# Kernel tuning notes

Hardware: AMD Instinct MI355X
Metric: run time of the kernel (lower is better)

The kernel has to match this reference:

```python
import jax, jax.numpy as jnp
import numpy as np

N = 1_600_000          # total points across all polylines
NUM_SEG = 100_000      # number of polylines (segments for scatter_max)
C_IN = 64
C_OUT = 64
NEG_SLOPE = 0.01       # F.leaky_relu default


def setup_inputs() -> dict:
    key = jax.random.key(0)
    k1, k2, k3, k4 = jax.random.split(key, 4)
    features = jax.random.normal(k1, (N, C_IN), dtype=jnp.float32)
    W = jax.random.normal(k2, (C_OUT, C_IN), dtype=jnp.float32) * (1.0 / np.sqrt(C_IN))
    b = jax.random.normal(k3, (C_OUT,), dtype=jnp.float32) * 0.01
    agg_indices = jax.random.randint(k4, (N,), 0, NUM_SEG, dtype=jnp.int32)
    return {"features": features, "W": W, "b": b, "agg_indices": agg_indices}


def reference(features, W, b, agg_indices):
    # fc: Linear(in_channels, out_channels)  -> [N, C_OUT]
    h = features @ W.T + b
    # leaky_relu (default negative_slope=0.01)
    h = jnp.where(h >= 0, h, NEG_SLOPE * h)
    # scatter_max over segments (dim=0): [NUM_SEG, C_OUT]
    agg = jax.ops.segment_max(h, agg_indices, num_segments=NUM_SEG)
    # guard against empty segments (-inf from segment_max); torch_scatter leaves them 0
    agg = jnp.where(jnp.isfinite(agg), agg, 0.0)
    # gather-broadcast and concat -> [N, 2*C_OUT]
    out = jnp.concatenate([h, agg[agg_indices]], axis=-1)
    return out, agg
```

## Files before the change

### kernel.cpp

```cpp
#include <hip/hip_runtime.h>
#include <stdint.h>

#define C 64
#define CAP 64

typedef __attribute__((ext_vector_type(8))) short short8v;
typedef __attribute__((ext_vector_type(4))) float f32x4;

static __device__ __forceinline__ short f2bf(float f) {
    unsigned u = __float_as_uint(f);
    unsigned r = (u + 0x7FFFu + ((u >> 16) & 1u)) >> 16;
    return (short)r;
}

static __device__ __forceinline__ short8v cvt8(f32x4 lo, f32x4 hi) {
    short8v v;
    v[0] = f2bf(lo[0]); v[1] = f2bf(lo[1]); v[2] = f2bf(lo[2]); v[3] = f2bf(lo[3]);
    v[4] = f2bf(hi[0]); v[5] = f2bf(hi[1]); v[6] = f2bf(hi[2]); v[7] = f2bf(hi[3]);
    return v;
}

__global__ __launch_bounds__(256) void k_gemm_fill(
    const float* __restrict__ feat, const float* __restrict__ W,
    const float* __restrict__ b, const int* __restrict__ idx,
    float* __restrict__ out, unsigned int* __restrict__ bucket, int N)
{
    const int lane = threadIdx.x & 63;
    const int gw   = blockIdx.x * (blockDim.x >> 6) + (threadIdx.x >> 6);
    const int nw   = gridDim.x * (blockDim.x >> 6);
    const int r    = lane & 15;
    const int q    = lane >> 4;

    short8v wf[4][2];
#pragma unroll
    for (int ct = 0; ct < 4; ++ct)
#pragma unroll
        for (int kh = 0; kh < 2; ++kh) {
            const float* src = W + (size_t)(ct * 16 + r) * C + kh * 32 + q * 8;
            wf[ct][kh] = cvt8(*(const f32x4*)src, *(const f32x4*)(src + 4));
        }
    float bias[4];
#pragma unroll
    for (int ct = 0; ct < 4; ++ct) bias[ct] = b[ct * 16 + r];

    const f32x4 zero = {0.f, 0.f, 0.f, 0.f};
    const int nTiles = N >> 5;

    for (int t = gw; t < nTiles; t += nw) {
        int rowid = t * 32 + lane;
        int seg   = (lane < 32) ? idx[rowid] : 0;

        const float* a0 = feat + ((size_t)t * 32 + r) * C + q * 8;
        const float* a1 = a0 + 16 * C;
        f32x4 l00 = *(const f32x4*)(a0);
        f32x4 l01 = *(const f32x4*)(a0 + 4);
        f32x4 l02 = *(const f32x4*)(a0 + 32);
        f32x4 l03 = *(const f32x4*)(a0 + 36);
        f32x4 l10 = *(const f32x4*)(a1);
        f32x4 l11 = *(const f32x4*)(a1 + 4);
        f32x4 l12 = *(const f32x4*)(a1 + 32);
        f32x4 l13 = *(const f32x4*)(a1 + 36);

        if (lane < 32) {
            unsigned int old = atomicAdd(&bucket[(size_t)seg * CAP], 1u);
            if (old < CAP - 1)
                bucket[(size_t)seg * CAP + 1 + old] = (unsigned int)rowid;
        }

        short8v A0k0 = cvt8(l00, l01), A0k1 = cvt8(l02, l03);
        short8v A1k0 = cvt8(l10, l11), A1k1 = cvt8(l12, l13);

        f32x4 d0[4], d1[4];
#pragma unroll
        for (int ct = 0; ct < 4; ++ct) {
            d0[ct] = __builtin_amdgcn_mfma_f32_16x16x32_bf16(A0k0, wf[ct][0], zero, 0, 0, 0);
            d0[ct] = __builtin_amdgcn_mfma_f32_16x16x32_bf16(A0k1, wf[ct][1], d0[ct], 0, 0, 0);
            d1[ct] = __builtin_amdgcn_mfma_f32_16x16x32_bf16(A1k0, wf[ct][0], zero, 0, 0, 0);
            d1[ct] = __builtin_amdgcn_mfma_f32_16x16x32_bf16(A1k1, wf[ct][1], d1[ct], 0, 0, 0);
        }

        const size_t row0 = (size_t)t * 32 + q * 4;
#pragma unroll
        for (int ct = 0; ct < 4; ++ct)
#pragma unroll
            for (int j = 0; j < 4; ++j) {
                float v0 = d0[ct][j] + bias[ct];
                v0 = fmaxf(v0, 0.01f * v0);
                out[(row0 + j) * (2 * C) + ct * 16 + r] = v0;
                float v1 = d1[ct][j] + bias[ct];
                v1 = fmaxf(v1, 0.01f * v1);
                out[(row0 + 16 + j) * (2 * C) + ct * 16 + r] = v1;
            }
    }
}

__global__ __launch_bounds__(256) void k_reduce_scatter(
    float* __restrict__ out, unsigned int* __restrict__ bucket, int nseg)
{
    const int lane = threadIdx.x & 63;
    const int seg  = blockIdx.x * (blockDim.x >> 6) + (threadIdx.x >> 6);
    if (seg >= nseg) return;

    unsigned int* brow = bucket + (size_t)seg * CAP;
    const unsigned int v = brow[lane];
    int cnt = __shfl((int)v, 0, 64);
    if (cnt > CAP - 1) cnt = CAP - 1;

    float acc = -INFINITY;
    for (int rr = 1; rr <= cnt; ++rr) {
        int row = __shfl((int)v, rr, 64);
        acc = fmaxf(acc, out[(size_t)row * (2 * C) + lane]);
    }
    if (cnt == 0) acc = 0.0f;

    ((float*)brow)[lane] = acc;

    for (int rr = 1; rr <= cnt; ++rr) {
        int row = __shfl((int)v, rr, 64);
        out[(size_t)row * (2 * C) + C + lane] = acc;
    }
}

extern "C" void kernel_launch(void* const* d_in, const int* in_sizes, int n_in,
                              void* d_out, int out_size, void* d_ws, size_t ws_size,
                              hipStream_t stream)
{
    (void)n_in; (void)d_ws; (void)ws_size;
    const float* feat = (const float*)d_in[0];
    const float* W    = (const float*)d_in[1];
    const float* b    = (const float*)d_in[2];
    const int*   idx  = (const int*)d_in[3];
    float* out = (float*)d_out;

    const int N    = in_sizes[0] / C;
    const int nseg = (out_size - N * 2 * C) / C;

    float* aggOut = out + (size_t)N * 2 * C;
    unsigned int* bucket = (unsigned int*)aggOut;

    hipMemsetAsync(aggOut, 0, (size_t)nseg * CAP * sizeof(unsigned int), stream);

    k_gemm_fill<<<2048, 256, 0, stream>>>(feat, W, b, idx, out, bucket, N);
    k_reduce_scatter<<<(nseg + 3) / 4, 256, 0, stream>>>(out, bucket, nseg);
}
```

Before: 471.8 us.

## Prefetch next GEMM tile, use nontemporal accesses, vectorize segment reduce with 4 rows per wave

The GEMM loop now software-prefetches the next tile's feature rows into registers while computing the current tile. Feature loads and output stores use nontemporal hints to limit cache pollution. The reduce/scatter kernel processes four rows per iteration, with each quarter-wave loading a float4 slice, and merges the partial maxima with xor shuffles. It then writes the broadcast aggregate as float4 stores. This cuts per-row load/store instruction count and latency, at the cost of more registers and redundant duplicate stores when the count is not a multiple of four.

```diff
diff --git a/kernel.cpp b/kernel.cpp
--- a/kernel.cpp
+++ b/kernel.cpp
@@ -19,6 +19,20 @@
     v[4] = f2bf(hi[0]); v[5] = f2bf(hi[1]); v[6] = f2bf(hi[2]); v[7] = f2bf(hi[3]);
     return v;
 }
+
+#define LOADA(t, L)                                                          \
+    {                                                                        \
+        const float* a0_ = feat + ((size_t)(t) * 32 + r) * C + q * 8;        \
+        const float* a1_ = a0_ + 16 * C;                                     \
+        L[0] = __builtin_nontemporal_load((const f32x4*)(a0_));              \
+        L[1] = __builtin_nontemporal_load((const f32x4*)(a0_ + 4));          \
+        L[2] = __builtin_nontemporal_load((const f32x4*)(a0_ + 32));         \
+        L[3] = __builtin_nontemporal_load((const f32x4*)(a0_ + 36));         \
+        L[4] = __builtin_nontemporal_load((const f32x4*)(a1_));              \
+        L[5] = __builtin_nontemporal_load((const f32x4*)(a1_ + 4));          \
+        L[6] = __builtin_nontemporal_load((const f32x4*)(a1_ + 32));         \
+        L[7] = __builtin_nontemporal_load((const f32x4*)(a1_ + 36));         \
+    }
 
 __global__ __launch_bounds__(256) void k_gemm_fill(
     const float* __restrict__ feat, const float* __restrict__ W,
@@ -46,20 +60,16 @@
     const f32x4 zero = {0.f, 0.f, 0.f, 0.f};
     const int nTiles = N >> 5;
 
-    for (int t = gw; t < nTiles; t += nw) {
-        int rowid = t * 32 + lane;
-        int seg   = (lane < 32) ? idx[rowid] : 0;
+    f32x4 cur[8], nxt[8];
+    int t = gw;
+    if (t < nTiles) LOADA(t, cur);
 
-        const float* a0 = feat + ((size_t)t * 32 + r) * C + q * 8;
-        const float* a1 = a0 + 16 * C;
-        f32x4 l00 = *(const f32x4*)(a0);
-        f32x4 l01 = *(const f32x4*)(a0 + 4);
-        f32x4 l02 = *(const f32x4*)(a0 + 32);
-        f32x4 l03 = *(const f32x4*)(a0 + 36);
-        f32x4 l10 = *(const f32x4*)(a1);
-        f32x4 l11 = *(const f32x4*)(a1 + 4);
-        f32x4 l12 = *(const f32x4*)(a1 + 32);
-        f32x4 l13 = *(const f32x4*)(a1 + 36);
+    for (; t < nTiles; t += nw) {
+        const int tn    = t + nw;
+        const int rowid = t * 32 + lane;
+        const int seg   = (lane < 32) ? idx[rowid] : 0;
+
+        if (tn < nTiles) LOADA(tn, nxt);
 
         if (lane < 32) {
             unsigned int old = atomicAdd(&bucket[(size_t)seg * CAP], 1u);
@@ -67,8 +77,8 @@
                 bucket[(size_t)seg * CAP + 1 + old] = (unsigned int)rowid;
         }
 
-        short8v A0k0 = cvt8(l00, l01), A0k1 = cvt8(l02, l03);
-        short8v A1k0 = cvt8(l10, l11), A1k1 = cvt8(l12, l13);
+        short8v A0k0 = cvt8(cur[0], cur[1]), A0k1 = cvt8(cur[2], cur[3]);
+        short8v A1k0 = cvt8(cur[4], cur[5]), A1k1 = cvt8(cur[6], cur[7]);
 
         f32x4 d0[4], d1[4];
 #pragma unroll
@@ -86,11 +96,14 @@
             for (int j = 0; j < 4; ++j) {
                 float v0 = d0[ct][j] + bias[ct];
                 v0 = fmaxf(v0, 0.01f * v0);
-                out[(row0 + j) * (2 * C) + ct * 16 + r] = v0;
+                __builtin_nontemporal_store(v0, &out[(row0 + j) * (2 * C) + ct * 16 + r]);
                 float v1 = d1[ct][j] + bias[ct];
                 v1 = fmaxf(v1, 0.01f * v1);
-                out[(row0 + 16 + j) * (2 * C) + ct * 16 + r] = v1;
+                __builtin_nontemporal_store(v1, &out[(row0 + 16 + j) * (2 * C) + ct * 16 + r]);
             }
+
+#pragma unroll
+        for (int i = 0; i < 8; ++i) cur[i] = nxt[i];
     }
 }
 
@@ -100,24 +113,49 @@
     const int lane = threadIdx.x & 63;
     const int seg  = blockIdx.x * (blockDim.x >> 6) + (threadIdx.x >> 6);
     if (seg >= nseg) return;
+    const int cq = lane >> 4;
+    const int cc = (lane & 15) * 4;
 
     unsigned int* brow = bucket + (size_t)seg * CAP;
     const unsigned int v = brow[lane];
     int cnt = __shfl((int)v, 0, 64);
     if (cnt > CAP - 1) cnt = CAP - 1;
 
-    float acc = -INFINITY;
-    for (int rr = 1; rr <= cnt; ++rr) {
-        int row = __shfl((int)v, rr, 64);
-        acc = fmaxf(acc, out[(size_t)row * (2 * C) + lane]);
+    const float ninf = -__builtin_inff();
+    f32x4 acc = {ninf, ninf, ninf, ninf};
+
+    const int ng = (cnt + 3) >> 2;
+    for (int g = 0; g < ng; ++g) {
+        int s    = 4 * g + cq;
+        int slot = (s < cnt) ? (1 + s) : 1;
+        int row  = __shfl((int)v, slot, 64);
+        const float* src = out + (size_t)row * (2 * C) + cc;
+        f32x4 hv = __builtin_nontemporal_load((const f32x4*)src);
+        acc[0] = fmaxf(acc[0], hv[0]);
+        acc[1] = fmaxf(acc[1], hv[1]);
+        acc[2] = fmaxf(acc[2], hv[2]);
+        acc[3] = fmaxf(acc[3], hv[3]);
     }
-    if (cnt == 0) acc = 0.0f;
 
-    ((float*)brow)[lane] = acc;
+#pragma unroll
+    for (int j = 0; j < 4; ++j) {
+        float o = __shfl_xor(acc[j], 16, 64);
+        acc[j] = fmaxf(acc[j], o);
+        o = __shfl_xor(acc[j], 32, 64);
+        acc[j] = fmaxf(acc[j], o);
+    }
 
-    for (int rr = 1; rr <= cnt; ++rr) {
-        int row = __shfl((int)v, rr, 64);
-        out[(size_t)row * (2 * C) + C + lane] = acc;
+    if (cnt == 0) { acc[0] = 0.f; acc[1] = 0.f; acc[2] = 0.f; acc[3] = 0.f; }
+
+    if (lane < 16)
+        *(f32x4*)((float*)brow + cc) = acc;
+
+    for (int g = 0; g < ng; ++g) {
+        int s    = 4 * g + cq;
+        int slot = (s < cnt) ? (1 + s) : 1;
+        int row  = __shfl((int)v, slot, 64);
+        float* dst = out + (size_t)row * (2 * C) + C + cc;
+        __builtin_nontemporal_store(acc, (f32x4*)dst);
     }
 }
 
```

After: 432.2 us. 8.4% less time.
